# Kernel optimization log

Measured on AMD Instinct MI355X. Metric: run time of the kernel, lower is better.

Reference implementation:

```python
import jax, jax.numpy as jnp
import numpy as np

N = 50000
E = 800000
F0, F1, F2 = 256, 128, 64
EPS = 1e-5


def setup_inputs() -> dict:
    key = jax.random.key(0)
    ks = jax.random.split(key, 20)
    x = jax.random.normal(ks[0], (N, F0), dtype=jnp.float32)
    src = jax.random.randint(ks[1], (E,), 0, N)
    dst = jax.random.randint(ks[2], (E,), 0, N)
    edge_index = jnp.stack([src, dst]).astype(jnp.int64)

    def lin(k, fi, fo):
        s = 1.0 / np.sqrt(fi)
        k1, k2 = jax.random.split(k)
        W = jax.random.uniform(k1, (fi, fo), minval=-s, maxval=s, dtype=jnp.float32)
        b = jax.random.uniform(k2, (fo,), minval=-s, maxval=s, dtype=jnp.float32)
        return W, b

    We1, be1 = lin(ks[3], F0, F1)
    We2, be2 = lin(ks[4], F1, F2)
    Wd1, bd1 = lin(ks[5], F2, F1)
    Wd2, bd2 = lin(ks[6], F1, F0)
    return {
        'x': x, 'edge_index': edge_index,
        'We1': We1, 'be1': be1, 'g1': jnp.ones((F1,)), 'bb1': jnp.zeros((F1,)),
        'We2': We2, 'be2': be2, 'g2': jnp.ones((F2,)), 'bb2': jnp.zeros((F2,)),
        'Wd1': Wd1, 'bd1': bd1, 'g3': jnp.ones((F1,)), 'bb3': jnp.zeros((F1,)),
        'Wd2': Wd2, 'bd2': bd2, 'g4': jnp.ones((F0,)), 'bb4': jnp.zeros((F0,)),
    }


def _gcn(x, W, b, src, dst, dinv_src_dst, dinv_self):
    # PyG GCNConv: linear first, then sym-normalized propagation with self-loops
    h = x @ W + b                               # [N, Fout]
    msg = h[src] * dinv_src_dst[:, None]        # [E, Fout]
    out = jax.ops.segment_sum(msg, dst, num_segments=N)
    return out + h * dinv_self[:, None]         # self-loop term


def _bn(x, g, b):
    # BatchNorm1d training-mode: biased batch stats over node dim
    m = jnp.mean(x, axis=0)
    v = jnp.mean(jnp.square(x - m), axis=0)
    return g * (x - m) * jax.lax.rsqrt(v + EPS) + b


def reference(x, edge_index, We1, be1, g1, bb1, We2, be2, g2, bb2,
              Wd1, bd1, g3, bb3, Wd2, bd2, g4, bb4):
    src, dst = edge_index[0], edge_index[1]
    deg = jnp.zeros((N,), x.dtype).at[dst].add(1.0) + 1.0  # in-degree + self-loop
    dinv = jax.lax.rsqrt(deg)
    dsd = dinv[src] * dinv[dst]
    dself = dinv * dinv

    relu = jax.nn.relu
    # Encoder block 0 (outer i==0): relu(GCN), relu(BN)
    h = relu(_gcn(x, We1, be1, src, dst, dsd, dself))
    h = relu(_bn(h, g1, bb1))
    enc1 = h
    # Encoder block 1 (outer i==1 == len(inner)-1): relu(GCN), BN (no relu)
    h = relu(_gcn(h, We2, be2, src, dst, dsd, dself))
    h = _bn(h, g2, bb2)
    enc2 = h
    # Decoder block 0: relu(GCN), relu(BN)
    h = relu(_gcn(h, Wd1, bd1, src, dst, dsd, dself))
    h = relu(_bn(h, g3, bb3))
    # Decoder block 1 (i==1): relu(GCN), BN (no relu)
    h = relu(_gcn(h, Wd2, bd2, src, dst, dsd, dself))
    h = _bn(h, g4, bb4)
    # AE returns (reconstruction, encoded_embeddings)
    return h, enc1, enc2
```

## Files before the change

### kernel.cpp

```cpp
#include <hip/hip_runtime.h>

#define N_NODES 50000
#define F0 256
#define F1 128
#define F2 64
#define BN_EPS 1e-5f

typedef float f32x4 __attribute__((ext_vector_type(4)));
typedef __bf16 bf16x8 __attribute__((ext_vector_type(8)));
typedef unsigned short ushort8v __attribute__((ext_vector_type(8)));

__device__ __forceinline__ float bflo(unsigned v) { return __uint_as_float(v << 16); }
__device__ __forceinline__ float bfhi(unsigned v) { return __uint_as_float(v & 0xFFFF0000u); }
__device__ __forceinline__ unsigned short f2bf(float f) {
  unsigned u = __float_as_uint(f);
  u += 0x7FFFu + ((u >> 16) & 1u);
  return (unsigned short)(u >> 16);
}
__device__ __forceinline__ void split2(float a, unsigned short& hi, unsigned short& lo) {
  hi = f2bf(a);
  float hf = __uint_as_float((unsigned)hi << 16);
  lo = f2bf(a - hf);
}
__device__ __forceinline__ int rdl(int v, int l) { return __builtin_amdgcn_readlane(v, l); }
__device__ __forceinline__ float rdlf(float v, int l) {
  return __uint_as_float((unsigned)__builtin_amdgcn_readlane(__float_as_int(v), l));
}

__global__ void count_dst(const int* __restrict__ dst, int* __restrict__ counts, int E) {
  int e = blockIdx.x * blockDim.x + threadIdx.x;
  if (e < E) atomicAdd(&counts[dst[e]], 1);
}

__global__ __launch_bounds__(256) void scan_blocks(const int* __restrict__ counts,
                                                   int* __restrict__ offs,
                                                   int* __restrict__ bsum,
                                                   float* __restrict__ dinv) {
  __shared__ int s_w[4];
  const int tid = threadIdx.x, lane = tid & 63, wid = tid >> 6;
  const int base = blockIdx.x * 1024 + tid * 4;
  int v0 = 0, v1 = 0, v2 = 0, v3 = 0;
  if (base + 3 < N_NODES) {
    int4 v = *(const int4*)(counts + base);
    v0 = v.x; v1 = v.y; v2 = v.z; v3 = v.w;
  } else if (base < N_NODES) {
    v0 = counts[base];
    if (base + 1 < N_NODES) v1 = counts[base + 1];
    if (base + 2 < N_NODES) v2 = counts[base + 2];
  }
  if (base < N_NODES) {
    dinv[base] = rsqrtf((float)v0 + 1.0f);
    if (base + 1 < N_NODES) dinv[base + 1] = rsqrtf((float)v1 + 1.0f);
    if (base + 2 < N_NODES) dinv[base + 2] = rsqrtf((float)v2 + 1.0f);
    if (base + 3 < N_NODES) dinv[base + 3] = rsqrtf((float)v3 + 1.0f);
  }
  int t = v0 + v1 + v2 + v3;
  int incl = t;
#pragma unroll
  for (int d = 1; d < 64; d <<= 1) {
    int x = __shfl_up(incl, d);
    if (lane >= d) incl += x;
  }
  if (lane == 63) s_w[wid] = incl;
  __syncthreads();
  int woff = 0;
#pragma unroll
  for (int j = 0; j < 4; j++)
    if (j < wid) woff += s_w[j];
  int p = woff + incl - t;
  if (base < N_NODES) offs[base] = p;
  p += v0;
  if (base + 1 < N_NODES) offs[base + 1] = p;
  p += v1;
  if (base + 2 < N_NODES) offs[base + 2] = p;
  p += v2;
  if (base + 3 < N_NODES) offs[base + 3] = p;
  if (tid == 255) bsum[blockIdx.x] = woff + incl;
}

__global__ void scan_tops(int* __restrict__ bsum, int* __restrict__ offs, int nblk) {
  int lane = threadIdx.x;
  int v = (lane < nblk) ? bsum[lane] : 0;
  int incl = v;
#pragma unroll
  for (int d = 1; d < 64; d <<= 1) {
    int x = __shfl_up(incl, d);
    if (lane >= d) incl += x;
  }
  if (lane < nblk) bsum[lane] = incl - v;
  if (lane == 63) offs[N_NODES] = incl;
}

__global__ __launch_bounds__(256) void scan_add(int* __restrict__ offs,
                                                const int* __restrict__ bsum) {
  const int add = bsum[blockIdx.x];
  const int base = blockIdx.x * 1024 + threadIdx.x * 4;
  if (base + 3 < N_NODES) {
    int4 v = *(const int4*)(offs + base);
    v.x += add; v.y += add; v.z += add; v.w += add;
    *(int4*)(offs + base) = v;
  } else if (base < N_NODES) {
    offs[base] += add;
    if (base + 1 < N_NODES) offs[base + 1] += add;
    if (base + 2 < N_NODES) offs[base + 2] += add;
  }
}

__global__ void fill_csr(const int* __restrict__ src, const int* __restrict__ dst,
                         const int* __restrict__ offs, int* __restrict__ cursor,
                         const float* __restrict__ dinv,
                         int* __restrict__ csr_src, float* __restrict__ csr_w, int E) {
  int e = blockIdx.x * blockDim.x + threadIdx.x;
  if (e < E) {
    int s = src[e], d = dst[e];
    int p = offs[d] + atomicAdd(&cursor[d], 1);
    csr_src[p] = s;
    csr_w[p] = dinv[s] * dinv[d];
  }
}

__global__ void compute_rowsum(const int* __restrict__ offs, const float* __restrict__ csr_w,
                               const float* __restrict__ dinv, float* __restrict__ rowsum) {
  int i = blockIdx.x * blockDim.x + threadIdx.x;
  if (i < N_NODES) {
    float s = dinv[i] * dinv[i];
    int e1 = offs[i + 1];
    for (int e = offs[i]; e < e1; e++) s += csr_w[e];
    rowsum[i] = s;
  }
}

__device__ __forceinline__ void wt_one(const float* W, unsigned short* Wh, unsigned short* Wl,
                                       int K, int N, int idx) {
  int k = idx / N, n = idx - k * N;
  unsigned short h, l;
  split2(W[idx], h, l);
  Wh[(size_t)n * K + k] = h;
  Wl[(size_t)n * K + k] = l;
}

__global__ void convert_weights(const float* __restrict__ We1, const float* __restrict__ We2,
                                const float* __restrict__ Wd1, const float* __restrict__ Wd2,
                                unsigned short* W1h, unsigned short* W1l,
                                unsigned short* W2h, unsigned short* W2l,
                                unsigned short* W3h, unsigned short* W3l,
                                unsigned short* W4h, unsigned short* W4l) {
  int idx = blockIdx.x * blockDim.x + threadIdx.x;
  if (idx < 32768) {
    wt_one(We1, W1h, W1l, 256, 128, idx);
  } else if (idx < 40960) {
    wt_one(We2, W2h, W2l, 128, 64, idx - 32768);
  } else if (idx < 49152) {
    wt_one(Wd1, W3h, W3l, 64, 128, idx - 40960);
  } else if (idx < 81920) {
    wt_one(Wd2, W4h, W4l, 128, 256, idx - 49152);
  }
}

template <int BN, bool STATS, bool AF32>
__global__ __launch_bounds__(256) void mfma_gemm_split(
    const unsigned short* __restrict__ Ahi, const unsigned short* __restrict__ Alo,
    const float* __restrict__ Af,
    const unsigned short* __restrict__ Whi, const unsigned short* __restrict__ Wlo,
    const float* __restrict__ bias, const float* __restrict__ rowsum,
    unsigned short* __restrict__ Cb, float* __restrict__ Cf,
    float* __restrict__ stat, int M, int K, int N) {
  constexpr int BM = 128;
  constexpr int MT = (BN == 128) ? 4 : 2;
  constexpr int NT = 4;
  __shared__ __align__(16) unsigned short AsH[4][BM][8];
  __shared__ __align__(16) unsigned short AsL[4][BM][8];
  __shared__ __align__(16) unsigned short BsH[4][BN][8];
  __shared__ __align__(16) unsigned short BsL[4][BN][8];
  const int tid = threadIdx.x;
  const int lane = tid & 63, wid = tid >> 6;
  const int quad = lane >> 4, ln = lane & 15;
  const int m0 = blockIdx.x * BM;
  const int n0 = blockIdx.y * BN;
  const int wm = (BN == 128) ? (wid & 1) * 64 : wid * 32;
  const int wn = (BN == 128) ? (wid >> 1) * 64 : 0;
  f32x4 acc[MT][NT] = {};

  const int arow = tid >> 2, aseg = tid & 3;
  for (int k0 = 0; k0 < K; k0 += 32) {
#pragma unroll
    for (int i = 0; i < 2; i++) {
      int row = arow + i * 64;
      int gm = m0 + row;
      if (AF32) {
        float4 u0 = make_float4(0.f, 0.f, 0.f, 0.f), u1 = u0;
        if (gm < M) {
          u0 = *(const float4*)(Af + (size_t)gm * K + k0 + aseg * 8);
          u1 = *(const float4*)(Af + (size_t)gm * K + k0 + aseg * 8 + 4);
        }
        ushort4 h0, l0, h1, l1;
        split2(u0.x, h0.x, l0.x); split2(u0.y, h0.y, l0.y);
        split2(u0.z, h0.z, l0.z); split2(u0.w, h0.w, l0.w);
        split2(u1.x, h1.x, l1.x); split2(u1.y, h1.y, l1.y);
        split2(u1.z, h1.z, l1.z); split2(u1.w, h1.w, l1.w);
        *(ushort4*)(&AsH[aseg][row][0]) = h0;
        *(ushort4*)(&AsH[aseg][row][4]) = h1;
        *(ushort4*)(&AsL[aseg][row][0]) = l0;
        *(ushort4*)(&AsL[aseg][row][4]) = l1;
      } else {
        ushort8v vh = {0, 0, 0, 0, 0, 0, 0, 0};
        ushort8v vl = {0, 0, 0, 0, 0, 0, 0, 0};
        if (gm < M) {
          vh = *(const ushort8v*)(Ahi + (size_t)gm * K + k0 + aseg * 8);
          vl = *(const ushort8v*)(Alo + (size_t)gm * K + k0 + aseg * 8);
        }
        *(ushort8v*)(&AsH[aseg][row][0]) = vh;
        *(ushort8v*)(&AsL[aseg][row][0]) = vl;
      }
    }
#pragma unroll
    for (int i = 0; i < BN / 64; i++) {
      int n = arow + i * 64;
      *(ushort8v*)(&BsH[aseg][n][0]) =
          *(const ushort8v*)(Whi + (size_t)(n0 + n) * K + k0 + aseg * 8);
      *(ushort8v*)(&BsL[aseg][n][0]) =
          *(const ushort8v*)(Wlo + (size_t)(n0 + n) * K + k0 + aseg * 8);
    }
    __syncthreads();
    bf16x8 ah[MT], al[MT], bh[NT], bl[NT];
#pragma unroll
    for (int mt = 0; mt < MT; mt++) {
      ah[mt] = *(const bf16x8*)(&AsH[quad][wm + mt * 16 + ln][0]);
      al[mt] = *(const bf16x8*)(&AsL[quad][wm + mt * 16 + ln][0]);
    }
#pragma unroll
    for (int nt = 0; nt < NT; nt++) {
      bh[nt] = *(const bf16x8*)(&BsH[quad][wn + nt * 16 + ln][0]);
      bl[nt] = *(const bf16x8*)(&BsL[quad][wn + nt * 16 + ln][0]);
    }
#pragma unroll
    for (int mt = 0; mt < MT; mt++)
#pragma unroll
      for (int nt = 0; nt < NT; nt++) {
        acc[mt][nt] = __builtin_amdgcn_mfma_f32_16x16x32_bf16(ah[mt], bl[nt], acc[mt][nt], 0, 0, 0);
        acc[mt][nt] = __builtin_amdgcn_mfma_f32_16x16x32_bf16(al[mt], bh[nt], acc[mt][nt], 0, 0, 0);
        acc[mt][nt] = __builtin_amdgcn_mfma_f32_16x16x32_bf16(ah[mt], bh[nt], acc[mt][nt], 0, 0, 0);
      }
    __syncthreads();
  }

  if (!STATS) {
#pragma unroll
    for (int nt = 0; nt < NT; nt++) {
      int gn = n0 + wn + nt * 16 + ln;
      float bv = bias[gn];
#pragma unroll
      for (int mt = 0; mt < MT; mt++) {
#pragma unroll
        for (int r = 0; r < 4; r++) {
          int gm = m0 + wm + mt * 16 + quad * 4 + r;
          if (gm < M) Cb[(size_t)gm * N + gn] = f2bf(acc[mt][nt][r] + bv);
        }
      }
    }
  } else {
    float rs[MT][4];
#pragma unroll
    for (int mt = 0; mt < MT; mt++)
#pragma unroll
      for (int r = 0; r < 4; r++) {
        int gm = m0 + wm + mt * 16 + quad * 4 + r;
        rs[mt][r] = (gm < M) ? rowsum[gm] : 0.f;
      }
#pragma unroll
    for (int nt = 0; nt < NT; nt++) {
      int gn = n0 + wn + nt * 16 + ln;
      float bv = bias[gn];
      float ls = 0.f, lq = 0.f;
#pragma unroll
      for (int mt = 0; mt < MT; mt++) {
#pragma unroll
        for (int r = 0; r < 4; r++) {
          int gm = m0 + wm + mt * 16 + quad * 4 + r;
          if (gm < M) {
            float v = fmaxf(fmaf(bv, rs[mt][r], acc[mt][nt][r]), 0.f);
            Cf[(size_t)gm * N + gn] = v;
            ls += v;
            lq = fmaf(v, v, lq);
          }
        }
      }
      ls += __shfl_xor(ls, 16); ls += __shfl_xor(ls, 32);
      lq += __shfl_xor(lq, 16); lq += __shfl_xor(lq, 32);
      if (quad == 0) {
        atomicAdd(&stat[gn], ls);
        atomicAdd(&stat[256 + gn], lq);
      }
    }
  }
}

template <bool RELU_STATS, bool OUT_SPLIT>
__global__ __launch_bounds__(256) void agg128_rl(
    const unsigned short* __restrict__ hb, const int* __restrict__ offs,
    const int* __restrict__ csr_src, const float* __restrict__ csr_w,
    const float* __restrict__ dinv, float* __restrict__ outf,
    unsigned short* __restrict__ outhi, unsigned short* __restrict__ outlo,
    float* __restrict__ stat) {
  const int tid = threadIdx.x;
  const int lane = tid & 63;
  const int widx = tid >> 6;
  const int half = lane >> 5;
  const int hl = lane & 31;
  const int nwaves = gridDim.x * 4;
  float ls0 = 0.f, ls1 = 0.f, ls2 = 0.f, ls3 = 0.f;
  float lq0 = 0.f, lq1 = 0.f, lq2 = 0.f, lq3 = 0.f;

  for (int node = blockIdx.x * 4 + widx; node < N_NODES; node += nwaves) {
    const int e0 = __builtin_amdgcn_readfirstlane(offs[node]);
    const int e1 = __builtin_amdgcn_readfirstlane(offs[node + 1]);
    float a0 = 0.f, a1 = 0.f, a2 = 0.f, a3 = 0.f;
    for (int e = e0; e < e1; e += 64) {
      const int cnt = min(64, e1 - e);
      int idx = 0;
      float wt = 0.f;
      if (lane < cnt) {
        idx = csr_src[e + lane];
        wt = csr_w[e + lane];
      }
      const int nb = (cnt + 15) & ~15;
      for (int j = 0; j < nb; j += 16) {
#pragma unroll
        for (int u = 0; u < 8; u++) {
          int sa = rdl(idx, j + 2 * u);
          int sb = rdl(idx, j + 2 * u + 1);
          float wa = rdlf(wt, j + 2 * u);
          float wb = rdlf(wt, j + 2 * u + 1);
          int s = half ? sb : sa;
          float w = half ? wb : wa;
          uint2 v = *(const uint2*)(hb + (size_t)s * 128 + hl * 4);
          a0 = fmaf(bflo(v.x), w, a0);
          a1 = fmaf(bfhi(v.x), w, a1);
          a2 = fmaf(bflo(v.y), w, a2);
          a3 = fmaf(bfhi(v.y), w, a3);
        }
      }
    }
    a0 += __shfl_xor(a0, 32);
    a1 += __shfl_xor(a1, 32);
    a2 += __shfl_xor(a2, 32);
    a3 += __shfl_xor(a3, 32);
    float di = dinv[node];
    float ds = di * di;
    uint2 vs = *(const uint2*)(hb + (size_t)node * 128 + hl * 4);
    a0 = fmaf(bflo(vs.x), ds, a0);
    a1 = fmaf(bfhi(vs.x), ds, a1);
    a2 = fmaf(bflo(vs.y), ds, a2);
    a3 = fmaf(bfhi(vs.y), ds, a3);
    if (RELU_STATS) {
      a0 = fmaxf(a0, 0.f);
      a1 = fmaxf(a1, 0.f);
      a2 = fmaxf(a2, 0.f);
      a3 = fmaxf(a3, 0.f);
      if (half == 0) {
        ls0 += a0; ls1 += a1; ls2 += a2; ls3 += a3;
        lq0 = fmaf(a0, a0, lq0);
        lq1 = fmaf(a1, a1, lq1);
        lq2 = fmaf(a2, a2, lq2);
        lq3 = fmaf(a3, a3, lq3);
      }
    }
    if (half == 0) {
      if (OUT_SPLIT) {
        unsigned short h0, l0, h1, l1, h2, l2, h3, l3;
        split2(a0, h0, l0);
        split2(a1, h1, l1);
        split2(a2, h2, l2);
        split2(a3, h3, l3);
        ushort4 hv, lv;
        hv.x = h0; hv.y = h1; hv.z = h2; hv.w = h3;
        lv.x = l0; lv.y = l1; lv.z = l2; lv.w = l3;
        *(ushort4*)(outhi + (size_t)node * 128 + hl * 4) = hv;
        *(ushort4*)(outlo + (size_t)node * 128 + hl * 4) = lv;
      } else {
        *(float4*)(outf + (size_t)node * 128 + hl * 4) = make_float4(a0, a1, a2, a3);
      }
    }
  }

  if (RELU_STATS) {
    __shared__ float red[4][128];
    if (half == 0) {
      red[widx][hl * 4 + 0] = ls0;
      red[widx][hl * 4 + 1] = ls1;
      red[widx][hl * 4 + 2] = ls2;
      red[widx][hl * 4 + 3] = ls3;
    }
    __syncthreads();
    if (tid < 128) {
      atomicAdd(&stat[tid], red[0][tid] + red[1][tid] + red[2][tid] + red[3][tid]);
    }
    __syncthreads();
    if (half == 0) {
      red[widx][hl * 4 + 0] = lq0;
      red[widx][hl * 4 + 1] = lq1;
      red[widx][hl * 4 + 2] = lq2;
      red[widx][hl * 4 + 3] = lq3;
    }
    __syncthreads();
    if (tid < 128) {
      atomicAdd(&stat[256 + tid], red[0][tid] + red[1][tid] + red[2][tid] + red[3][tid]);
    }
  }
}

template <bool RELU_STATS, bool OUT_SPLIT>
__global__ __launch_bounds__(256) void agg64_rl(
    const unsigned short* __restrict__ hb, const int* __restrict__ offs,
    const int* __restrict__ csr_src, const float* __restrict__ csr_w,
    const float* __restrict__ dinv, float* __restrict__ outf,
    unsigned short* __restrict__ outhi, unsigned short* __restrict__ outlo,
    float* __restrict__ stat) {
  const int tid = threadIdx.x;
  const int lane = tid & 63;
  const int widx = tid >> 6;
  const int ql = lane & 15;
  const int nwaves = gridDim.x * 4;
  float ls0 = 0.f, ls1 = 0.f, ls2 = 0.f, ls3 = 0.f;
  float lq0 = 0.f, lq1 = 0.f, lq2 = 0.f, lq3 = 0.f;

  for (int node = blockIdx.x * 4 + widx; node < N_NODES; node += nwaves) {
    const int e0 = __builtin_amdgcn_readfirstlane(offs[node]);
    const int e1 = __builtin_amdgcn_readfirstlane(offs[node + 1]);
    float a0 = 0.f, a1 = 0.f, a2 = 0.f, a3 = 0.f;
    for (int e = e0; e < e1; e += 64) {
      const int cnt = min(64, e1 - e);
      int idx = 0;
      float wt = 0.f;
      if (lane < cnt) {
        idx = csr_src[e + lane];
        wt = csr_w[e + lane];
      }
      const int nb = (cnt + 31) & ~31;
      for (int j = 0; j < nb; j += 32) {
#pragma unroll
        for (int u = 0; u < 8; u++) {
          int s0 = rdl(idx, j + 4 * u + 0);
          int s1 = rdl(idx, j + 4 * u + 1);
          int s2 = rdl(idx, j + 4 * u + 2);
          int s3 = rdl(idx, j + 4 * u + 3);
          float w0 = rdlf(wt, j + 4 * u + 0);
          float w1 = rdlf(wt, j + 4 * u + 1);
          float w2 = rdlf(wt, j + 4 * u + 2);
          float w3 = rdlf(wt, j + 4 * u + 3);
          int sx = (lane & 16) ? s1 : s0;
          int sy = (lane & 16) ? s3 : s2;
          int s = (lane & 32) ? sy : sx;
          float wx = (lane & 16) ? w1 : w0;
          float wy = (lane & 16) ? w3 : w2;
          float w = (lane & 32) ? wy : wx;
          uint2 v = *(const uint2*)(hb + (size_t)s * 64 + ql * 4);
          a0 = fmaf(bflo(v.x), w, a0);
          a1 = fmaf(bfhi(v.x), w, a1);
          a2 = fmaf(bflo(v.y), w, a2);
          a3 = fmaf(bfhi(v.y), w, a3);
        }
      }
    }
    a0 += __shfl_xor(a0, 16); a0 += __shfl_xor(a0, 32);
    a1 += __shfl_xor(a1, 16); a1 += __shfl_xor(a1, 32);
    a2 += __shfl_xor(a2, 16); a2 += __shfl_xor(a2, 32);
    a3 += __shfl_xor(a3, 16); a3 += __shfl_xor(a3, 32);
    float di = dinv[node];
    float ds = di * di;
    uint2 vs = *(const uint2*)(hb + (size_t)node * 64 + ql * 4);
    a0 = fmaf(bflo(vs.x), ds, a0);
    a1 = fmaf(bfhi(vs.x), ds, a1);
    a2 = fmaf(bflo(vs.y), ds, a2);
    a3 = fmaf(bfhi(vs.y), ds, a3);
    if (RELU_STATS) {
      a0 = fmaxf(a0, 0.f);
      a1 = fmaxf(a1, 0.f);
      a2 = fmaxf(a2, 0.f);
      a3 = fmaxf(a3, 0.f);
      if (lane < 16) {
        ls0 += a0; ls1 += a1; ls2 += a2; ls3 += a3;
        lq0 = fmaf(a0, a0, lq0);
        lq1 = fmaf(a1, a1, lq1);
        lq2 = fmaf(a2, a2, lq2);
        lq3 = fmaf(a3, a3, lq3);
      }
    }
    if (lane < 16) {
      if (OUT_SPLIT) {
        unsigned short h0, l0, h1, l1, h2, l2, h3, l3;
        split2(a0, h0, l0);
        split2(a1, h1, l1);
        split2(a2, h2, l2);
        split2(a3, h3, l3);
        ushort4 hv, lv;
        hv.x = h0; hv.y = h1; hv.z = h2; hv.w = h3;
        lv.x = l0; lv.y = l1; lv.z = l2; lv.w = l3;
        *(ushort4*)(outhi + (size_t)node * 64 + ql * 4) = hv;
        *(ushort4*)(outlo + (size_t)node * 64 + ql * 4) = lv;
      } else {
        *(float4*)(outf + (size_t)node * 64 + ql * 4) = make_float4(a0, a1, a2, a3);
      }
    }
  }

  if (RELU_STATS) {
    __shared__ float red[4][64];
    if (lane < 16) {
      red[widx][ql * 4 + 0] = ls0;
      red[widx][ql * 4 + 1] = ls1;
      red[widx][ql * 4 + 2] = ls2;
      red[widx][ql * 4 + 3] = ls3;
    }
    __syncthreads();
    if (tid < 64) {
      atomicAdd(&stat[tid], red[0][tid] + red[1][tid] + red[2][tid] + red[3][tid]);
    }
    __syncthreads();
    if (lane < 16) {
      red[widx][ql * 4 + 0] = lq0;
      red[widx][ql * 4 + 1] = lq1;
      red[widx][ql * 4 + 2] = lq2;
      red[widx][ql * 4 + 3] = lq3;
    }
    __syncthreads();
    if (tid < 64) {
      atomicAdd(&stat[256 + tid], red[0][tid] + red[1][tid] + red[2][tid] + red[3][tid]);
    }
  }
}

template <int F, bool RELU, bool WF32, bool WB16, bool WSPLIT>
__global__ __launch_bounds__(256) void bn_apply_f(const float* __restrict__ a,
                                                  const float* __restrict__ stat,
                                                  const float* __restrict__ g,
                                                  const float* __restrict__ bb,
                                                  float* __restrict__ outf,
                                                  unsigned short* __restrict__ outb,
                                                  unsigned short* __restrict__ outhi,
                                                  unsigned short* __restrict__ outlo) {
  __shared__ float s_scale[F], s_shift[F];
  const int tid = threadIdx.x;
  if (tid < F) {
    const float invN = 1.0f / (float)N_NODES;
    float mean = stat[tid] * invN;
    float var = fmaxf(stat[256 + tid] * invN - mean * mean, 0.f);
    float inv = rsqrtf(var + BN_EPS);
    float sc = g[tid] * inv;
    s_scale[tid] = sc;
    s_shift[tid] = bb[tid] - mean * sc;
  }
  __syncthreads();
  constexpr int C4 = F / 4;
  const int total = N_NODES * C4;
  for (int idx = blockIdx.x * blockDim.x + tid; idx < total; idx += gridDim.x * blockDim.x) {
    int c4 = idx % C4;
    float4 v = ((const float4*)a)[idx];
    float4 s = *(float4*)&s_scale[c4 * 4];
    float4 sh = *(float4*)&s_shift[c4 * 4];
    float4 o;
    o.x = fmaf(v.x, s.x, sh.x);
    o.y = fmaf(v.y, s.y, sh.y);
    o.z = fmaf(v.z, s.z, sh.z);
    o.w = fmaf(v.w, s.w, sh.w);
    if (RELU) {
      o.x = fmaxf(o.x, 0.f);
      o.y = fmaxf(o.y, 0.f);
      o.z = fmaxf(o.z, 0.f);
      o.w = fmaxf(o.w, 0.f);
    }
    if (WF32) ((float4*)outf)[idx] = o;
    if (WB16) {
      ushort4 b;
      b.x = f2bf(o.x); b.y = f2bf(o.y); b.z = f2bf(o.z); b.w = f2bf(o.w);
      ((ushort4*)outb)[idx] = b;
    }
    if (WSPLIT) {
      ushort4 h, l;
      split2(o.x, h.x, l.x);
      split2(o.y, h.y, l.y);
      split2(o.z, h.z, l.z);
      split2(o.w, h.w, l.w);
      ((ushort4*)outhi)[idx] = h;
      ((ushort4*)outlo)[idx] = l;
    }
  }
}

extern "C" void kernel_launch(void* const* d_in, const int* in_sizes, int n_in,
                              void* d_out, int out_size, void* d_ws, size_t ws_size,
                              hipStream_t stream) {
  const float* x = (const float*)d_in[0];
  const int* ei = (const int*)d_in[1];
  const int E = in_sizes[1] / 2;
  const int* src = ei;
  const int* dst = ei + E;
  const float* We1 = (const float*)d_in[2];  const float* be1 = (const float*)d_in[3];
  const float* g1  = (const float*)d_in[4];  const float* bb1 = (const float*)d_in[5];
  const float* We2 = (const float*)d_in[6];  const float* be2 = (const float*)d_in[7];
  const float* g2  = (const float*)d_in[8];  const float* bb2 = (const float*)d_in[9];
  const float* Wd1 = (const float*)d_in[10]; const float* bd1 = (const float*)d_in[11];
  const float* g3  = (const float*)d_in[12]; const float* bb3 = (const float*)d_in[13];
  const float* Wd2 = (const float*)d_in[14]; const float* bd2 = (const float*)d_in[15];
  const float* g4  = (const float*)d_in[16]; const float* bb4 = (const float*)d_in[17];

  float* out = (float*)d_out;
  char* ws = (char*)d_ws;
  unsigned short* A0b  = (unsigned short*)(ws + 0);
  unsigned short* A1b  = (unsigned short*)(ws + 12800000);
  unsigned short* C2b  = (unsigned short*)(ws + 32000000);
  unsigned short* G3hi = (unsigned short*)(ws + 0);
  unsigned short* G3lo = (unsigned short*)(ws + 6400000);
  unsigned short* D3b  = (unsigned short*)(ws + 12800000);
  unsigned short* G4hi = (unsigned short*)(ws + 0);
  unsigned short* G4lo = (unsigned short*)(ws + 25600000);
  unsigned short* Wb   = (unsigned short*)(ws + 48000000);
  unsigned short* W1h = Wb;            unsigned short* W1l = W1h + 32768;
  unsigned short* W2h = W1l + 32768;   unsigned short* W2l = W2h + 8192;
  unsigned short* W3h = W2l + 8192;    unsigned short* W3l = W3h + 8192;
  unsigned short* W4h = W3l + 8192;    unsigned short* W4l = W4h + 32768;
  float* B0f  = (float*)(ws + 51200000);
  int*   csrS   = (int*)(ws + 102400000);
  float* csrW   = (float*)(ws + 105600000);
  float* stat4  = (float*)(ws + 108800000);
  int*   bsum   = (int*)(ws + 108808192);
  int*   counts = (int*)(ws + 108810000);
  int*   cursor = (int*)(ws + 109010000);
  int*   offs   = (int*)(ws + 109210000);
  float* dinv   = (float*)(ws + 109410064);
  if (ws_size < 109604160) return;
  float* rowsum = (float*)cursor;

  float* enc1 = out + (size_t)N_NODES * F0;
  float* enc2 = enc1 + (size_t)N_NODES * F1;

  const int EB = (E + 255) / 256;
  const int AGG_GRID = 2048;
  const int MB = (N_NODES + 127) / 128;
  const int SCAN_B = (N_NODES + 1023) / 1024;

  convert_weights<<<320, 256, 0, stream>>>(We1, We2, Wd1, Wd2, W1h, W1l, W2h, W2l,
                                           W3h, W3l, W4h, W4l);
  hipMemsetAsync(counts, 0, 2 * N_NODES * sizeof(int) + 20000, stream);
  hipMemsetAsync(stat4, 0, 4 * 512 * sizeof(float), stream);
  count_dst<<<EB, 256, 0, stream>>>(dst, counts, E);
  scan_blocks<<<SCAN_B, 256, 0, stream>>>(counts, offs, bsum, dinv);
  scan_tops<<<1, 64, 0, stream>>>(bsum, offs, SCAN_B);
  scan_add<<<SCAN_B, 256, 0, stream>>>(offs, bsum);
  fill_csr<<<EB, 256, 0, stream>>>(src, dst, offs, cursor, dinv, csrS, csrW, E);
  compute_rowsum<<<(N_NODES + 255) / 256, 256, 0, stream>>>(offs, csrW, dinv, rowsum);

  mfma_gemm_split<128, false, true><<<dim3(MB, 1), 256, 0, stream>>>(
      nullptr, nullptr, x, W1h, W1l, be1, nullptr, A0b, nullptr, nullptr, N_NODES, F0, F1);
  agg128_rl<true, false><<<AGG_GRID, 256, 0, stream>>>(
      A0b, offs, csrS, csrW, dinv, B0f, nullptr, nullptr, stat4);
  bn_apply_f<F1, true, true, false, false><<<2048, 256, 0, stream>>>(
      B0f, stat4, g1, bb1, enc1, nullptr, nullptr, nullptr);

  mfma_gemm_split<64, false, true><<<dim3(MB, 1), 256, 0, stream>>>(
      nullptr, nullptr, enc1, W2h, W2l, be2, nullptr, A1b, nullptr, nullptr, N_NODES, F1, F2);
  agg64_rl<true, false><<<AGG_GRID, 256, 0, stream>>>(
      A1b, offs, csrS, csrW, dinv, B0f, nullptr, nullptr, stat4 + 512);
  bn_apply_f<F2, false, true, true, false><<<2048, 256, 0, stream>>>(
      B0f, stat4 + 512, g2, bb2, enc2, C2b, nullptr, nullptr);

  agg64_rl<false, true><<<AGG_GRID, 256, 0, stream>>>(
      C2b, offs, csrS, csrW, dinv, nullptr, G3hi, G3lo, nullptr);
  mfma_gemm_split<128, true, false><<<dim3(MB, 1), 256, 0, stream>>>(
      G3hi, G3lo, nullptr, W3h, W3l, bd1, rowsum, nullptr, B0f, stat4 + 1024, N_NODES, F2, F1);
  bn_apply_f<F1, true, false, true, false><<<2048, 256, 0, stream>>>(
      B0f, stat4 + 1024, g3, bb3, nullptr, D3b, nullptr, nullptr);

  agg128_rl<false, true><<<AGG_GRID, 256, 0, stream>>>(
      D3b, offs, csrS, csrW, dinv, nullptr, G4hi, G4lo, nullptr);
  mfma_gemm_split<128, true, false><<<dim3(MB, 2), 256, 0, stream>>>(
      G4hi, G4lo, nullptr, W4h, W4l, bd2, rowsum, nullptr, B0f, stat4 + 1536, N_NODES, F1, F0);
  bn_apply_f<F0, false, true, false, false><<<2048, 256, 0, stream>>>(
      B0f, stat4 + 1536, g4, bb4, out, nullptr, nullptr, nullptr);
}
```

Measured before the change: 642.6 us.

## Restructure aggregation to 8-edge slots with two interleaved nodes per wave; fuse rowsum

```diff
diff --git a/kernel.cpp b/kernel.cpp
--- a/kernel.cpp
+++ b/kernel.cpp
@@ -21,10 +21,6 @@
   hi = f2bf(a);
   float hf = __uint_as_float((unsigned)hi << 16);
   lo = f2bf(a - hf);
-}
-__device__ __forceinline__ int rdl(int v, int l) { return __builtin_amdgcn_readlane(v, l); }
-__device__ __forceinline__ float rdlf(float v, int l) {
-  return __uint_as_float((unsigned)__builtin_amdgcn_readlane(__float_as_int(v), l));
 }
 
 __global__ void count_dst(const int* __restrict__ dst, int* __restrict__ counts, int E) {
@@ -92,41 +88,41 @@
 }
 
 __global__ __launch_bounds__(256) void scan_add(int* __restrict__ offs,
-                                                const int* __restrict__ bsum) {
+                                                const int* __restrict__ bsum,
+                                                const float* __restrict__ dinv,
+                                                float* __restrict__ rowsum) {
   const int add = bsum[blockIdx.x];
   const int base = blockIdx.x * 1024 + threadIdx.x * 4;
   if (base + 3 < N_NODES) {
     int4 v = *(const int4*)(offs + base);
     v.x += add; v.y += add; v.z += add; v.w += add;
     *(int4*)(offs + base) = v;
+    float4 d = *(const float4*)(dinv + base);
+    float4 r;
+    r.x = d.x * d.x; r.y = d.y * d.y; r.z = d.z * d.z; r.w = d.w * d.w;
+    *(float4*)(rowsum + base) = r;
   } else if (base < N_NODES) {
-    offs[base] += add;
-    if (base + 1 < N_NODES) offs[base + 1] += add;
-    if (base + 2 < N_NODES) offs[base + 2] += add;
+    for (int k = 0; k < 4 && base + k < N_NODES; k++) {
+      offs[base + k] += add;
+      float d = dinv[base + k];
+      rowsum[base + k] = d * d;
+    }
   }
 }
 
 __global__ void fill_csr(const int* __restrict__ src, const int* __restrict__ dst,
                          const int* __restrict__ offs, int* __restrict__ cursor,
                          const float* __restrict__ dinv,
-                         int* __restrict__ csr_src, float* __restrict__ csr_w, int E) {
+                         int* __restrict__ csr_src, float* __restrict__ csr_w,
+                         float* __restrict__ rowsum, int E) {
   int e = blockIdx.x * blockDim.x + threadIdx.x;
   if (e < E) {
     int s = src[e], d = dst[e];
     int p = offs[d] + atomicAdd(&cursor[d], 1);
+    float w = dinv[s] * dinv[d];
     csr_src[p] = s;
-    csr_w[p] = dinv[s] * dinv[d];
-  }
-}
-
-__global__ void compute_rowsum(const int* __restrict__ offs, const float* __restrict__ csr_w,
-                               const float* __restrict__ dinv, float* __restrict__ rowsum) {
-  int i = blockIdx.x * blockDim.x + threadIdx.x;
-  if (i < N_NODES) {
-    float s = dinv[i] * dinv[i];
-    int e1 = offs[i + 1];
-    for (int e = offs[i]; e < e1; e++) s += csr_w[e];
-    rowsum[i] = s;
+    csr_w[p] = w;
+    atomicAdd(&rowsum[d], w);
   }
 }
 
@@ -295,8 +291,80 @@
   }
 }
 
+
+__device__ __forceinline__ void agg64_pass(const unsigned short* __restrict__ hb,
+                                           const int* __restrict__ csr_src,
+                                           const float* __restrict__ csr_w,
+                                           int e, int e1, int chunk, float (&a)[8]) {
+  int s = 0;
+  float w = 0.f;
+  if (e < e1) {
+    s = csr_src[e];
+    w = csr_w[e];
+  }
+  const uint4 v = *(const uint4*)(hb + (size_t)s * 64 + chunk * 8);
+  a[0] = fmaf(bflo(v.x), w, a[0]);
+  a[1] = fmaf(bfhi(v.x), w, a[1]);
+  a[2] = fmaf(bflo(v.y), w, a[2]);
+  a[3] = fmaf(bfhi(v.y), w, a[3]);
+  a[4] = fmaf(bflo(v.z), w, a[4]);
+  a[5] = fmaf(bfhi(v.z), w, a[5]);
+  a[6] = fmaf(bflo(v.w), w, a[6]);
+  a[7] = fmaf(bfhi(v.w), w, a[7]);
+}
+
 template <bool RELU_STATS, bool OUT_SPLIT>
-__global__ __launch_bounds__(256) void agg128_rl(
+__device__ __forceinline__ void agg64_fin(const unsigned short* __restrict__ hb,
+                                          const float* __restrict__ dinv, int node, int slot,
+                                          int chunk, float (&a)[8], float (&ls)[8],
+                                          float (&lq)[8], float* __restrict__ outf,
+                                          unsigned short* __restrict__ outhi,
+                                          unsigned short* __restrict__ outlo) {
+#pragma unroll
+  for (int i = 0; i < 8; i++) {
+    a[i] += __shfl_xor(a[i], 8);
+    a[i] += __shfl_xor(a[i], 16);
+    a[i] += __shfl_xor(a[i], 32);
+  }
+  if (slot != 0) return;
+  float di = dinv[node];
+  float ds = di * di;
+  const uint4 vs = *(const uint4*)(hb + (size_t)node * 64 + chunk * 8);
+  a[0] = fmaf(bflo(vs.x), ds, a[0]);
+  a[1] = fmaf(bfhi(vs.x), ds, a[1]);
+  a[2] = fmaf(bflo(vs.y), ds, a[2]);
+  a[3] = fmaf(bfhi(vs.y), ds, a[3]);
+  a[4] = fmaf(bflo(vs.z), ds, a[4]);
+  a[5] = fmaf(bfhi(vs.z), ds, a[5]);
+  a[6] = fmaf(bflo(vs.w), ds, a[6]);
+  a[7] = fmaf(bfhi(vs.w), ds, a[7]);
+  if (RELU_STATS) {
+#pragma unroll
+    for (int i = 0; i < 8; i++) {
+      a[i] = fmaxf(a[i], 0.f);
+      ls[i] += a[i];
+      lq[i] = fmaf(a[i], a[i], lq[i]);
+    }
+  }
+  if (OUT_SPLIT) {
+    ushort8v hv, lv;
+#pragma unroll
+    for (int i = 0; i < 8; i++) {
+      unsigned short h, l;
+      split2(a[i], h, l);
+      hv[i] = h;
+      lv[i] = l;
+    }
+    *(ushort8v*)(outhi + (size_t)node * 64 + chunk * 8) = hv;
+    *(ushort8v*)(outlo + (size_t)node * 64 + chunk * 8) = lv;
+  } else {
+    *(float4*)(outf + (size_t)node * 64 + chunk * 8) = make_float4(a[0], a[1], a[2], a[3]);
+    *(float4*)(outf + (size_t)node * 64 + chunk * 8 + 4) = make_float4(a[4], a[5], a[6], a[7]);
+  }
+}
+
+template <bool RELU_STATS, bool OUT_SPLIT>
+__global__ __launch_bounds__(256) void agg64_sc(
     const unsigned short* __restrict__ hb, const int* __restrict__ offs,
     const int* __restrict__ csr_src, const float* __restrict__ csr_w,
     const float* __restrict__ dinv, float* __restrict__ outf,
@@ -305,112 +373,164 @@
   const int tid = threadIdx.x;
   const int lane = tid & 63;
   const int widx = tid >> 6;
-  const int half = lane >> 5;
-  const int hl = lane & 31;
+  const int slot = lane >> 3;
+  const int chunk = lane & 7;
   const int nwaves = gridDim.x * 4;
-  float ls0 = 0.f, ls1 = 0.f, ls2 = 0.f, ls3 = 0.f;
-  float lq0 = 0.f, lq1 = 0.f, lq2 = 0.f, lq3 = 0.f;
-
-  for (int node = blockIdx.x * 4 + widx; node < N_NODES; node += nwaves) {
-    const int e0 = __builtin_amdgcn_readfirstlane(offs[node]);
-    const int e1 = __builtin_amdgcn_readfirstlane(offs[node + 1]);
-    float a0 = 0.f, a1 = 0.f, a2 = 0.f, a3 = 0.f;
-    for (int e = e0; e < e1; e += 64) {
-      const int cnt = min(64, e1 - e);
-      int idx = 0;
-      float wt = 0.f;
-      if (lane < cnt) {
-        idx = csr_src[e + lane];
-        wt = csr_w[e + lane];
-      }
-      const int nb = (cnt + 15) & ~15;
-      for (int j = 0; j < nb; j += 16) {
-#pragma unroll
-        for (int u = 0; u < 8; u++) {
-          int sa = rdl(idx, j + 2 * u);
-          int sb = rdl(idx, j + 2 * u + 1);
-          float wa = rdlf(wt, j + 2 * u);
-          float wb = rdlf(wt, j + 2 * u + 1);
-          int s = half ? sb : sa;
-          float w = half ? wb : wa;
-          uint2 v = *(const uint2*)(hb + (size_t)s * 128 + hl * 4);
-          a0 = fmaf(bflo(v.x), w, a0);
-          a1 = fmaf(bfhi(v.x), w, a1);
-          a2 = fmaf(bflo(v.y), w, a2);
-          a3 = fmaf(bfhi(v.y), w, a3);
-        }
-      }
-    }
-    a0 += __shfl_xor(a0, 32);
-    a1 += __shfl_xor(a1, 32);
-    a2 += __shfl_xor(a2, 32);
-    a3 += __shfl_xor(a3, 32);
-    float di = dinv[node];
-    float ds = di * di;
-    uint2 vs = *(const uint2*)(hb + (size_t)node * 128 + hl * 4);
-    a0 = fmaf(bflo(vs.x), ds, a0);
-    a1 = fmaf(bfhi(vs.x), ds, a1);
-    a2 = fmaf(bflo(vs.y), ds, a2);
-    a3 = fmaf(bfhi(vs.y), ds, a3);
-    if (RELU_STATS) {
-      a0 = fmaxf(a0, 0.f);
-      a1 = fmaxf(a1, 0.f);
-      a2 = fmaxf(a2, 0.f);
-      a3 = fmaxf(a3, 0.f);
-      if (half == 0) {
-        ls0 += a0; ls1 += a1; ls2 += a2; ls3 += a3;
-        lq0 = fmaf(a0, a0, lq0);
-        lq1 = fmaf(a1, a1, lq1);
-        lq2 = fmaf(a2, a2, lq2);
-        lq3 = fmaf(a3, a3, lq3);
-      }
-    }
-    if (half == 0) {
-      if (OUT_SPLIT) {
-        unsigned short h0, l0, h1, l1, h2, l2, h3, l3;
-        split2(a0, h0, l0);
-        split2(a1, h1, l1);
-        split2(a2, h2, l2);
-        split2(a3, h3, l3);
-        ushort4 hv, lv;
-        hv.x = h0; hv.y = h1; hv.z = h2; hv.w = h3;
-        lv.x = l0; lv.y = l1; lv.z = l2; lv.w = l3;
-        *(ushort4*)(outhi + (size_t)node * 128 + hl * 4) = hv;
-        *(ushort4*)(outlo + (size_t)node * 128 + hl * 4) = lv;
-      } else {
-        *(float4*)(outf + (size_t)node * 128 + hl * 4) = make_float4(a0, a1, a2, a3);
-      }
-    }
+  float ls[8] = {}, lq[8] = {};
+
+  for (int base = blockIdx.x * 4 + widx; base < N_NODES; base += 2 * nwaves) {
+    const int nA = base;
+    const int nB = base + nwaves;
+    const bool hasB = (nB < N_NODES);
+    const int eA0 = __builtin_amdgcn_readfirstlane(offs[nA]);
+    const int eA1 = __builtin_amdgcn_readfirstlane(offs[nA + 1]);
+    int eB0 = 0, eB1 = 0;
+    if (hasB) {
+      eB0 = __builtin_amdgcn_readfirstlane(offs[nB]);
+      eB1 = __builtin_amdgcn_readfirstlane(offs[nB + 1]);
+    }
+    float aA[8] = {}, aB[8] = {};
+    int ebA = eA0, ebB = eB0;
+    while (ebA < eA1 || ebB < eB1) {
+      if (ebA < eA1) {
+        agg64_pass(hb, csr_src, csr_w, ebA + slot, eA1, chunk, aA);
+        agg64_pass(hb, csr_src, csr_w, ebA + 8 + slot, eA1, chunk, aA);
+      }
+      if (ebB < eB1) {
+        agg64_pass(hb, csr_src, csr_w, ebB + slot, eB1, chunk, aB);
+        agg64_pass(hb, csr_src, csr_w, ebB + 8 + slot, eB1, chunk, aB);
+      }
+      ebA += 16;
+      ebB += 16;
+    }
+    agg64_fin<RELU_STATS, OUT_SPLIT>(hb, dinv, nA, slot, chunk, aA, ls, lq, outf, outhi, outlo);
+    if (hasB)
+      agg64_fin<RELU_STATS, OUT_SPLIT>(hb, dinv, nB, slot, chunk, aB, ls, lq, outf, outhi, outlo);
   }
 
   if (RELU_STATS) {
-    __shared__ float red[4][128];
-    if (half == 0) {
-      red[widx][hl * 4 + 0] = ls0;
-      red[widx][hl * 4 + 1] = ls1;
-      red[widx][hl * 4 + 2] = ls2;
-      red[widx][hl * 4 + 3] = ls3;
+    __shared__ float red[4][64];
+    if (slot == 0) {
+#pragma unroll
+      for (int i = 0; i < 8; i++) red[widx][chunk * 8 + i] = ls[i];
     }
     __syncthreads();
-    if (tid < 128) {
+    if (tid < 64) {
       atomicAdd(&stat[tid], red[0][tid] + red[1][tid] + red[2][tid] + red[3][tid]);
     }
     __syncthreads();
-    if (half == 0) {
-      red[widx][hl * 4 + 0] = lq0;
-      red[widx][hl * 4 + 1] = lq1;
-      red[widx][hl * 4 + 2] = lq2;
-      red[widx][hl * 4 + 3] = lq3;
+    if (slot == 0) {
+#pragma unroll
+      for (int i = 0; i < 8; i++) red[widx][chunk * 8 + i] = lq[i];
     }
     __syncthreads();
-    if (tid < 128) {
+    if (tid < 64) {
       atomicAdd(&stat[256 + tid], red[0][tid] + red[1][tid] + red[2][tid] + red[3][tid]);
     }
   }
 }
 
+__device__ __forceinline__ void agg128_pass(const unsigned short* __restrict__ hb,
+                                            const int* __restrict__ csr_src,
+                                            const float* __restrict__ csr_w,
+                                            int e, int e1, int chunk, float (&a)[16]) {
+  int s = 0;
+  float w = 0.f;
+  if (e < e1) {
+    s = csr_src[e];
+    w = csr_w[e];
+  }
+  const unsigned short* p = hb + (size_t)s * 128 + chunk * 8;
+  const uint4 v0 = *(const uint4*)(p);
+  const uint4 v1 = *(const uint4*)(p + 64);
+  a[0] = fmaf(bflo(v0.x), w, a[0]);
+  a[1] = fmaf(bfhi(v0.x), w, a[1]);
+  a[2] = fmaf(bflo(v0.y), w, a[2]);
+  a[3] = fmaf(bfhi(v0.y), w, a[3]);
+  a[4] = fmaf(bflo(v0.z), w, a[4]);
+  a[5] = fmaf(bfhi(v0.z), w, a[5]);
+  a[6] = fmaf(bflo(v0.w), w, a[6]);
+  a[7] = fmaf(bfhi(v0.w), w, a[7]);
+  a[8] = fmaf(bflo(v1.x), w, a[8]);
+  a[9] = fmaf(bfhi(v1.x), w, a[9]);
+  a[10] = fmaf(bflo(v1.y), w, a[10]);
+  a[11] = fmaf(bfhi(v1.y), w, a[11]);
+  a[12] = fmaf(bflo(v1.z), w, a[12]);
+  a[13] = fmaf(bfhi(v1.z), w, a[13]);
+  a[14] = fmaf(bflo(v1.w), w, a[14]);
+  a[15] = fmaf(bfhi(v1.w), w, a[15]);
+}
+
 template <bool RELU_STATS, bool OUT_SPLIT>
-__global__ __launch_bounds__(256) void agg64_rl(
+__device__ __forceinline__ void agg128_fin(const unsigned short* __restrict__ hb,
+                                           const float* __restrict__ dinv, int node, int slot,
+                                           int chunk, float (&a)[16], float (&ls)[16],
+                                           float (&lq)[16], float* __restrict__ outf,
+                                           unsigned short* __restrict__ outhi,
+                                           unsigned short* __restrict__ outlo) {
+#pragma unroll
+  for (int i = 0; i < 16; i++) {
+    a[i] += __shfl_xor(a[i], 8);
+    a[i] += __shfl_xor(a[i], 16);
+    a[i] += __shfl_xor(a[i], 32);
+  }
+  if (slot != 0) return;
+  float di = dinv[node];
+  float ds = di * di;
+  const unsigned short* p = hb + (size_t)node * 128 + chunk * 8;
+  const uint4 v0 = *(const uint4*)(p);
+  const uint4 v1 = *(const uint4*)(p + 64);
+  a[0] = fmaf(bflo(v0.x), ds, a[0]);
+  a[1] = fmaf(bfhi(v0.x), ds, a[1]);
+  a[2] = fmaf(bflo(v0.y), ds, a[2]);
+  a[3] = fmaf(bfhi(v0.y), ds, a[3]);
+  a[4] = fmaf(bflo(v0.z), ds, a[4]);
+  a[5] = fmaf(bfhi(v0.z), ds, a[5]);
+  a[6] = fmaf(bflo(v0.w), ds, a[6]);
+  a[7] = fmaf(bfhi(v0.w), ds, a[7]);
+  a[8] = fmaf(bflo(v1.x), ds, a[8]);
+  a[9] = fmaf(bfhi(v1.x), ds, a[9]);
+  a[10] = fmaf(bflo(v1.y), ds, a[10]);
+  a[11] = fmaf(bfhi(v1.y), ds, a[11]);
+  a[12] = fmaf(bflo(v1.z), ds, a[12]);
+  a[13] = fmaf(bfhi(v1.z), ds, a[13]);
+  a[14] = fmaf(bflo(v1.w), ds, a[14]);
+  a[15] = fmaf(bfhi(v1.w), ds, a[15]);
+  if (RELU_STATS) {
+#pragma unroll
+    for (int i = 0; i < 16; i++) {
+      a[i] = fmaxf(a[i], 0.f);
+      ls[i] += a[i];
+      lq[i] = fmaf(a[i], a[i], lq[i]);
+    }
+  }
+  if (OUT_SPLIT) {
+    ushort8v hv0, lv0, hv1, lv1;
+#pragma unroll
+    for (int i = 0; i < 8; i++) {
+      unsigned short h, l;
+      split2(a[i], h, l);
+      hv0[i] = h;
+      lv0[i] = l;
+      split2(a[8 + i], h, l);
+      hv1[i] = h;
+      lv1[i] = l;
+    }
+    *(ushort8v*)(outhi + (size_t)node * 128 + chunk * 8) = hv0;
+    *(ushort8v*)(outhi + (size_t)node * 128 + 64 + chunk * 8) = hv1;
+    *(ushort8v*)(outlo + (size_t)node * 128 + chunk * 8) = lv0;
+    *(ushort8v*)(outlo + (size_t)node * 128 + 64 + chunk * 8) = lv1;
+  } else {
+    *(float4*)(outf + (size_t)node * 128 + chunk * 8) = make_float4(a[0], a[1], a[2], a[3]);
+    *(float4*)(outf + (size_t)node * 128 + chunk * 8 + 4) = make_float4(a[4], a[5], a[6], a[7]);
+    *(float4*)(outf + (size_t)node * 128 + 64 + chunk * 8) = make_float4(a[8], a[9], a[10], a[11]);
+    *(float4*)(outf + (size_t)node * 128 + 64 + chunk * 8 + 4) =
+        make_float4(a[12], a[13], a[14], a[15]);
+  }
+}
+
+template <bool RELU_STATS, bool OUT_SPLIT>
+__global__ __launch_bounds__(256) void agg128_sc(
     const unsigned short* __restrict__ hb, const int* __restrict__ offs,
     const int* __restrict__ csr_src, const float* __restrict__ csr_w,
     const float* __restrict__ dinv, float* __restrict__ outf,
@@ -419,112 +539,64 @@
   const int tid = threadIdx.x;
   const int lane = tid & 63;
   const int widx = tid >> 6;
-  const int ql = lane & 15;
+  const int slot = lane >> 3;
+  const int chunk = lane & 7;
   const int nwaves = gridDim.x * 4;
-  float ls0 = 0.f, ls1 = 0.f, ls2 = 0.f, ls3 = 0.f;
-  float lq0 = 0.f, lq1 = 0.f, lq2 = 0.f, lq3 = 0.f;
-
-  for (int node = blockIdx.x * 4 + widx; node < N_NODES; node += nwaves) {
-    const int e0 = __builtin_amdgcn_readfirstlane(offs[node]);
-    const int e1 = __builtin_amdgcn_readfirstlane(offs[node + 1]);
-    float a0 = 0.f, a1 = 0.f, a2 = 0.f, a3 = 0.f;
-    for (int e = e0; e < e1; e += 64) {
-      const int cnt = min(64, e1 - e);
-      int idx = 0;
-      float wt = 0.f;
-      if (lane < cnt) {
-        idx = csr_src[e + lane];
-        wt = csr_w[e + lane];
-      }
-      const int nb = (cnt + 31) & ~31;
-      for (int j = 0; j < nb; j += 32) {
-#pragma unroll
-        for (int u = 0; u < 8; u++) {
-          int s0 = rdl(idx, j + 4 * u + 0);
-          int s1 = rdl(idx, j + 4 * u + 1);
-          int s2 = rdl(idx, j + 4 * u + 2);
-          int s3 = rdl(idx, j + 4 * u + 3);
-          float w0 = rdlf(wt, j + 4 * u + 0);
-          float w1 = rdlf(wt, j + 4 * u + 1);
-          float w2 = rdlf(wt, j + 4 * u + 2);
-          float w3 = rdlf(wt, j + 4 * u + 3);
-          int sx = (lane & 16) ? s1 : s0;
-          int sy = (lane & 16) ? s3 : s2;
-          int s = (lane & 32) ? sy : sx;
-          float wx = (lane & 16) ? w1 : w0;
-          float wy = (lane & 16) ? w3 : w2;
-          float w = (lane & 32) ? wy : wx;
-          uint2 v = *(const uint2*)(hb + (size_t)s * 64 + ql * 4);
-          a0 = fmaf(bflo(v.x), w, a0);
-          a1 = fmaf(bfhi(v.x), w, a1);
-          a2 = fmaf(bflo(v.y), w, a2);
-          a3 = fmaf(bfhi(v.y), w, a3);
-        }
-      }
-    }
-    a0 += __shfl_xor(a0, 16); a0 += __shfl_xor(a0, 32);
-    a1 += __shfl_xor(a1, 16); a1 += __shfl_xor(a1, 32);
-    a2 += __shfl_xor(a2, 16); a2 += __shfl_xor(a2, 32);
-    a3 += __shfl_xor(a3, 16); a3 += __shfl_xor(a3, 32);
-    float di = dinv[node];
-    float ds = di * di;
-    uint2 vs = *(const uint2*)(hb + (size_t)node * 64 + ql * 4);
-    a0 = fmaf(bflo(vs.x), ds, a0);
-    a1 = fmaf(bfhi(vs.x), ds, a1);
-    a2 = fmaf(bflo(vs.y), ds, a2);
-    a3 = fmaf(bfhi(vs.y), ds, a3);
-    if (RELU_STATS) {
-      a0 = fmaxf(a0, 0.f);
-      a1 = fmaxf(a1, 0.f);
-      a2 = fmaxf(a2, 0.f);
-      a3 = fmaxf(a3, 0.f);
-      if (lane < 16) {
-        ls0 += a0; ls1 += a1; ls2 += a2; ls3 += a3;
-        lq0 = fmaf(a0, a0, lq0);
-        lq1 = fmaf(a1, a1, lq1);
-        lq2 = fmaf(a2, a2, lq2);
-        lq3 = fmaf(a3, a3, lq3);
-      }
-    }
-    if (lane < 16) {
-      if (OUT_SPLIT) {
-        unsigned short h0, l0, h1, l1, h2, l2, h3, l3;
-        split2(a0, h0, l0);
-        split2(a1, h1, l1);
-        split2(a2, h2, l2);
-        split2(a3, h3, l3);
-        ushort4 hv, lv;
-        hv.x = h0; hv.y = h1; hv.z = h2; hv.w = h3;
-        lv.x = l0; lv.y = l1; lv.z = l2; lv.w = l3;
-        *(ushort4*)(outhi + (size_t)node * 64 + ql * 4) = hv;
-        *(ushort4*)(outlo + (size_t)node * 64 + ql * 4) = lv;
-      } else {
-        *(float4*)(outf + (size_t)node * 64 + ql * 4) = make_float4(a0, a1, a2, a3);
-      }
-    }
+  float ls[16] = {}, lq[16] = {};
+
+  for (int base = blockIdx.x * 4 + widx; base < N_NODES; base += 2 * nwaves) {
+    const int nA = base;
+    const int nB = base + nwaves;
+    const bool hasB = (nB < N_NODES);
+    const int eA0 = __builtin_amdgcn_readfirstlane(offs[nA]);
+    const int eA1 = __builtin_amdgcn_readfirstlane(offs[nA + 1]);
+    int eB0 = 0, eB1 = 0;
+    if (hasB) {
+      eB0 = __builtin_amdgcn_readfirstlane(offs[nB]);
+      eB1 = __builtin_amdgcn_readfirstlane(offs[nB + 1]);
+    }
+    float aA[16] = {}, aB[16] = {};
+    int ebA = eA0, ebB = eB0;
+    while (ebA < eA1 || ebB < eB1) {
+      if (ebA < eA1) {
+        agg128_pass(hb, csr_src, csr_w, ebA + slot, eA1, chunk, aA);
+        agg128_pass(hb, csr_src, csr_w, ebA + 8 + slot, eA1, chunk, aA);
+      }
+      if (ebB < eB1) {
+        agg128_pass(hb, csr_src, csr_w, ebB + slot, eB1, chunk, aB);
+        agg128_pass(hb, csr_src, csr_w, ebB + 8 + slot, eB1, chunk, aB);
+      }
+      ebA += 16;
+      ebB += 16;
+    }
+    agg128_fin<RELU_STATS, OUT_SPLIT>(hb, dinv, nA, slot, chunk, aA, ls, lq, outf, outhi, outlo);
+    if (hasB)
+      agg128_fin<RELU_STATS, OUT_SPLIT>(hb, dinv, nB, slot, chunk, aB, ls, lq, outf, outhi, outlo);
   }
 
   if (RELU_STATS) {
-    __shared__ float red[4][64];
-    if (lane < 16) {
-      red[widx][ql * 4 + 0] = ls0;
-      red[widx][ql * 4 + 1] = ls1;
-      red[widx][ql * 4 + 2] = ls2;
-      red[widx][ql * 4 + 3] = ls3;
+    __shared__ float red[4][128];
+    if (slot == 0) {
+#pragma unroll
+      for (int i = 0; i < 8; i++) {
+        red[widx][chunk * 8 + i] = ls[i];
+        red[widx][64 + chunk * 8 + i] = ls[8 + i];
+      }
     }
     __syncthreads();
-    if (tid < 64) {
+    if (tid < 128) {
       atomicAdd(&stat[tid], red[0][tid] + red[1][tid] + red[2][tid] + red[3][tid]);
     }
     __syncthreads();
-    if (lane < 16) {
-      red[widx][ql * 4 + 0] = lq0;
-      red[widx][ql * 4 + 1] = lq1;
-      red[widx][ql * 4 + 2] = lq2;
-      red[widx][ql * 4 + 3] = lq3;
+    if (slot == 0) {
+#pragma unroll
+      for (int i = 0; i < 8; i++) {
+        red[widx][chunk * 8 + i] = lq[i];
+        red[widx][64 + chunk * 8 + i] = lq[8 + i];
+      }
     }
     __syncthreads();
-    if (tid < 64) {
+    if (tid < 128) {
       atomicAdd(&stat[256 + tid], red[0][tid] + red[1][tid] + red[2][tid] + red[3][tid]);
     }
   }
@@ -629,7 +701,7 @@
   int*   offs   = (int*)(ws + 109210000);
   float* dinv   = (float*)(ws + 109410064);
   if (ws_size < 109604160) return;
-  float* rowsum = (float*)cursor;
+  float* rowsum = (float*)counts;
 
   float* enc1 = out + (size_t)N_NODES * F0;
   float* enc2 = enc1 + (size_t)N_NODES * F1;
@@ -641,37 +713,36 @@
 
   convert_weights<<<320, 256, 0, stream>>>(We1, We2, Wd1, Wd2, W1h, W1l, W2h, W2l,
                                            W3h, W3l, W4h, W4l);
-  hipMemsetAsync(counts, 0, 2 * N_NODES * sizeof(int) + 20000, stream);
+  hipMemsetAsync(counts, 0, 400000, stream);
   hipMemsetAsync(stat4, 0, 4 * 512 * sizeof(float), stream);
   count_dst<<<EB, 256, 0, stream>>>(dst, counts, E);
   scan_blocks<<<SCAN_B, 256, 0, stream>>>(counts, offs, bsum, dinv);
   scan_tops<<<1, 64, 0, stream>>>(bsum, offs, SCAN_B);
-  scan_add<<<SCAN_B, 256, 0, stream>>>(offs, bsum);
-  fill_csr<<<EB, 256, 0, stream>>>(src, dst, offs, cursor, dinv, csrS, csrW, E);
-  compute_rowsum<<<(N_NODES + 255) / 256, 256, 0, stream>>>(offs, csrW, dinv, rowsum);
+  scan_add<<<SCAN_B, 256, 0, stream>>>(offs, bsum, dinv, rowsum);
+  fill_csr<<<EB, 256, 0, stream>>>(src, dst, offs, cursor, dinv, csrS, csrW, rowsum, E);
 
   mfma_gemm_split<128, false, true><<<dim3(MB, 1), 256, 0, stream>>>(
       nullptr, nullptr, x, W1h, W1l, be1, nullptr, A0b, nullptr, nullptr, N_NODES, F0, F1);
-  agg128_rl<true, false><<<AGG_GRID, 256, 0, stream>>>(
+  agg128_sc<true, false><<<AGG_GRID, 256, 0, stream>>>(
       A0b, offs, csrS, csrW, dinv, B0f, nullptr, nullptr, stat4);
   bn_apply_f<F1, true, true, false, false><<<2048, 256, 0, stream>>>(
       B0f, stat4, g1, bb1, enc1, nullptr, nullptr, nullptr);
 
   mfma_gemm_split<64, false, true><<<dim3(MB, 1), 256, 0, stream>>>(
       nullptr, nullptr, enc1, W2h, W2l, be2, nullptr, A1b, nullptr, nullptr, N_NODES, F1, F2);
-  agg64_rl<true, false><<<AGG_GRID, 256, 0, stream>>>(
+  agg64_sc<true, false><<<AGG_GRID, 256, 0, stream>>>(
       A1b, offs, csrS, csrW, dinv, B0f, nullptr, nullptr, stat4 + 512);
   bn_apply_f<F2, false, true, true, false><<<2048, 256, 0, stream>>>(
       B0f, stat4 + 512, g2, bb2, enc2, C2b, nullptr, nullptr);
 
-  agg64_rl<false, true><<<AGG_GRID, 256, 0, stream>>>(
+  agg64_sc<false, true><<<AGG_GRID, 256, 0, stream>>>(
       C2b, offs, csrS, csrW, dinv, nullptr, G3hi, G3lo, nullptr);
   mfma_gemm_split<128, true, false><<<dim3(MB, 1), 256, 0, stream>>>(
       G3hi, G3lo, nullptr, W3h, W3l, bd1, rowsum, nullptr, B0f, stat4 + 1024, N_NODES, F2, F1);
   bn_apply_f<F1, true, false, true, false><<<2048, 256, 0, stream>>>(
       B0f, stat4 + 1024, g3, bb3, nullptr, D3b, nullptr, nullptr);
 
-  agg128_rl<false, true><<<AGG_GRID, 256, 0, stream>>>(
+  agg128_sc<false, true><<<AGG_GRID, 256, 0, stream>>>(
       D3b, offs, csrS, csrW, dinv, nullptr, G4hi, G4lo, nullptr);
   mfma_gemm_split<128, true, false><<<dim3(MB, 2), 256, 0, stream>>>(
       G4hi, G4lo, nullptr, W4h, W4l, bd2, rowsum, nullptr, B0f, stat4 + 1536, N_NODES, F1, F0);
```

New measurement: 663.1 us. +3.2%, slower.
